# Performance work log

Measured on AMD Instinct MI355X. Metric: run time of the kernel, lower is better.

The kernel has to match this reference:

```python
import jax, jax.numpy as jnp
import numpy as np

BN_EPS = 1e-5


def grid_sample_bilinear(img, grid):
    """Torch F.grid_sample, mode=bilinear, padding_mode=zeros, align_corners=False.
    img: (B, C, H, W); grid: (B, N, 2) in [-1, 1] -> (B, C, N)."""
    B, C, H, W = img.shape
    x = ((grid[..., 0] + 1.0) * W - 1.0) * 0.5  # (B, N) pixel coords
    y = ((grid[..., 1] + 1.0) * H - 1.0) * 0.5
    x0 = jnp.floor(x)
    y0 = jnp.floor(y)
    x1 = x0 + 1.0
    y1 = y0 + 1.0
    wx1 = x - x0
    wx0 = 1.0 - wx1
    wy1 = y - y0
    wy0 = 1.0 - wy1
    img_flat = img.reshape(B, C, H * W)

    def corner(xi, yi, w):
        valid = (xi >= 0) & (xi <= W - 1) & (yi >= 0) & (yi <= H - 1)
        xi_c = jnp.clip(xi, 0, W - 1).astype(jnp.int32)
        yi_c = jnp.clip(yi, 0, H - 1).astype(jnp.int32)
        idx = yi_c * W + xi_c  # (B, N)
        vals = jnp.take_along_axis(img_flat, idx[:, None, :], axis=2)  # (B, C, N)
        return vals * (w * valid.astype(img.dtype))[:, None, :]

    return (corner(x0, y0, wx0 * wy0) + corner(x1, y0, wx1 * wy0)
            + corner(x0, y1, wx0 * wy1) + corner(x1, y1, wx1 * wy1))


def conv1x1(x, w, b):
    # x: (B, Cin, N), w: (Cout, Cin), b: (Cout,)
    return jnp.einsum('oi,bin->bon', w, x) + b[None, :, None]


def batchnorm1d_train(x, gamma, beta):
    # training-mode BN over (batch, length) per channel, biased variance
    mean = jnp.mean(x, axis=(0, 2), keepdims=True)
    var = jnp.mean((x - mean) ** 2, axis=(0, 2), keepdims=True)
    xn = (x - mean) * jax.lax.rsqrt(var + BN_EPS)
    return xn * gamma[None, :, None] + beta[None, :, None]


def setup_inputs() -> dict:
    key = jax.random.key(0)
    ks = jax.random.split(key, 12)
    B, N, CI, CP, H, W, R = 4, 16384, 256, 256, 64, 160, 4
    Cin = CI + CP
    Cb = CP // R

    def glorot(k, shape):
        fan_in = shape[1]
        return jax.random.normal(k, shape, dtype=jnp.float32) * (1.0 / np.sqrt(fan_in))

    return {
        'pts_img': jax.random.uniform(ks[0], (B, N, 2), dtype=jnp.float32, minval=-1.0, maxval=1.0),
        'img_feats': jax.random.normal(ks[1], (B, CI, H, W), dtype=jnp.float32),
        'pts_feats': jax.random.normal(ks[2], (B, CP, N), dtype=jnp.float32),
        'fusion_w': glorot(ks[3], (CP, Cin)),
        'fusion_b': jax.random.normal(ks[4], (CP,), dtype=jnp.float32) * 0.01,
        'bn_gamma': jnp.ones((CP,), dtype=jnp.float32),
        'bn_beta': jnp.zeros((CP,), dtype=jnp.float32),
        'ca1_w': glorot(ks[5], (Cb, CP)),
        'ca1_b': jax.random.normal(ks[6], (Cb,), dtype=jnp.float32) * 0.01,
        'ca2_w': glorot(ks[7], (CP, Cb)),
        'ca2_b': jax.random.normal(ks[8], (CP,), dtype=jnp.float32) * 0.01,
        'sa_w': glorot(ks[9], (Cb, CP)),
        'sa_b': jax.random.normal(ks[10], (Cb,), dtype=jnp.float32) * 0.01,
    }


def reference(pts_img, img_feats, pts_feats, fusion_w, fusion_b, bn_gamma, bn_beta,
              ca1_w, ca1_b, ca2_w, ca2_b, sa_w, sa_b):
    # grid_sample gather: (B, C_I, N)
    pts_wise_img_feats = grid_sample_bilinear(img_feats, pts_img)
    fusion = jnp.concatenate([pts_wise_img_feats, pts_feats], axis=1)  # (B, C_I+C_P, N)
    # fusion MLP: conv1x1 + BN + ReLU
    fusion = jax.nn.relu(batchnorm1d_train(conv1x1(fusion, fusion_w, fusion_b), bn_gamma, bn_beta))
    # spatial attention: max over channels of bottleneck conv, sigmoid gate
    spatial = jax.nn.sigmoid(jnp.max(conv1x1(fusion, sa_w, sa_b), axis=1, keepdims=True))
    fusion = spatial * fusion
    # channel attention: bottleneck MLP, global max-pool over points, sigmoid gate
    ca = conv1x1(jax.nn.relu(conv1x1(fusion, ca1_w, ca1_b)), ca2_w, ca2_b)  # (B, C_P, N)
    channel = jax.nn.sigmoid(jnp.max(ca, axis=2, keepdims=True))  # (B, C_P, 1)
    return channel * fusion
```

## Files before the change

### kernel.cpp

```cpp
#include <hip/hip_runtime.h>
#include <stdint.h>


typedef __attribute__((ext_vector_type(8))) short bf16x8;
typedef __attribute__((ext_vector_type(4))) float f32x4;

#define B_ 4
#define N_ 16384
#define H_ 64
#define W_ 160
#define HW_ (H_ * W_)
#define K_ 512

__device__ __forceinline__ float bf2f(unsigned short u) {
    union { unsigned int i; float f; } c; c.i = ((unsigned int)u) << 16; return c.f;
}
__device__ __forceinline__ unsigned short f2bf(float f) {
    union { float f; unsigned int i; } c; c.f = f;
    unsigned int u = c.i;
    return (unsigned short)((u + 0x7FFFu + ((u >> 16) & 1u)) >> 16);
}
__device__ __forceinline__ unsigned int fkey(float f) {
    union { float f; unsigned int u; int i; } c; c.f = f;
    return (c.i < 0) ? ~c.u : (c.u | 0x80000000u);
}
__device__ __forceinline__ float funkey(unsigned int k) {
    union { unsigned int u; float f; } c;
    c.u = (k & 0x80000000u) ? (k & 0x7FFFFFFFu) : ~k;
    return c.f;
}

__device__ __forceinline__ void async_copy16(void* lds, const void* g) {
#if defined(__has_builtin) && __has_builtin(__builtin_amdgcn_global_load_lds)
    __builtin_amdgcn_global_load_lds(
        (const __attribute__((address_space(1))) unsigned int*)g,
        (__attribute__((address_space(3))) unsigned int*)lds, 16, 0, 0);
#else
    *(uint4*)lds = *(const uint4*)g;
#endif
}

__global__ __launch_bounds__(256) void k_init(const float* __restrict__ fw,
                                              const float* __restrict__ saw,
                                              const float* __restrict__ c1w,
                                              const float* __restrict__ c2w,
                                              unsigned short* WfB, unsigned short* saB,
                                              unsigned short* ca1B, unsigned short* ca2B,
                                              float* buckets, unsigned int* camax) {
    int t = threadIdx.x;
    int j = blockIdx.x;
    if (j == 0) {
        for (int i = t; i < 16 * 512; i += 256) buckets[i] = 0.f;
        for (int i = t; i < 8 * 1024; i += 256) camax[i] = 0u;
    }
    int i = j * 256 + t;
    if (i < 131072) WfB[i] = f2bf(fw[i]);
    else if (i < 147456) saB[i - 131072] = f2bf(saw[i - 131072]);
    else if (i < 163840) ca1B[i - 147456] = f2bf(c1w[i - 147456]);
    else if (i < 180224) ca2B[i - 163840] = f2bf(c2w[i - 163840]);
}

__global__ __launch_bounds__(256, 3) void k_zimg(const unsigned short* __restrict__ WfB,
                                                 const float* __restrict__ img,
                                                 unsigned short* __restrict__ ZT) {
    __shared__ __align__(16) char smem[21504];
    unsigned short* At = (unsigned short*)smem;
    unsigned short* Bt = (unsigned short*)(smem + 16384);

    int t = threadIdx.x;
    int hw0 = blockIdx.x * 64, b = blockIdx.y;
    int w = t >> 6, lane = t & 63, quad = lane >> 4, l15 = lane & 15;

    const f32x4 fzero = {0.f, 0.f, 0.f, 0.f};
    f32x4 acc[4][4];
#pragma unroll
    for (int i = 0; i < 4; ++i)
#pragma unroll
        for (int j = 0; j < 4; ++j) acc[i][j] = fzero;

    for (int kt = 0; kt < 8; ++kt) {
        int k0 = kt * 32;
        __syncthreads();
#pragma unroll
        for (int q = 0; q < 4; ++q) {
            int row = q * 64 + (t >> 2);
            async_copy16(At + (size_t)q * 2048 + (size_t)t * 8,
                         WfB + (size_t)row * K_ + k0 + (t & 3) * 8);
        }
        {
            int c_local = t & 31, g = t >> 5;
            int c = k0 + c_local;
            const float* src = img + ((size_t)b * 256 + c) * (size_t)HW_ + hw0 + g * 8;
            float4 v0 = *(const float4*)(src + 0);
            float4 v1 = *(const float4*)(src + 4);
            unsigned short* dst = Bt + (size_t)(g * 8) * 40 + c_local;
            dst[0 * 40] = f2bf(v0.x); dst[1 * 40] = f2bf(v0.y);
            dst[2 * 40] = f2bf(v0.z); dst[3 * 40] = f2bf(v0.w);
            dst[4 * 40] = f2bf(v1.x); dst[5 * 40] = f2bf(v1.y);
            dst[6 * 40] = f2bf(v1.z); dst[7 * 40] = f2bf(v1.w);
        }
        __syncthreads();
        bf16x8 af[4], bv[4];
#pragma unroll
        for (int j = 0; j < 4; ++j)
            bv[j] = *(const bf16x8*)(Bt + (j * 16 + l15) * 40 + quad * 8);
#pragma unroll
        for (int i = 0; i < 4; ++i)
            af[i] = *(const bf16x8*)(At + (w * 64 + i * 16 + l15) * 32 + quad * 8);
#pragma unroll
        for (int i = 0; i < 4; ++i)
#pragma unroll
            for (int j = 0; j < 4; ++j)
                acc[i][j] = __builtin_amdgcn_mfma_f32_16x16x32_bf16(af[i], bv[j], acc[i][j], 0, 0, 0);
    }

    unsigned short* Zb = ZT + ((size_t)b * HW_ + hw0) * 256;
#pragma unroll
    for (int i = 0; i < 4; ++i) {
        int m = w * 64 + i * 16 + quad * 4;
#pragma unroll
        for (int j = 0; j < 4; ++j) {
            int n = j * 16 + l15;
            ushort4 o;
            o.x = f2bf(acc[i][j][0]);
            o.y = f2bf(acc[i][j][1]);
            o.z = f2bf(acc[i][j][2]);
            o.w = f2bf(acc[i][j][3]);
            *(ushort4*)(Zb + (size_t)n * 256 + m) = o;
        }
    }
}

__global__ __launch_bounds__(256, 2) void k_gemm1p(const unsigned short* __restrict__ WfB,
                                                   const float* __restrict__ pim,
                                                   const unsigned short* __restrict__ ZT,
                                                   const float* __restrict__ pts,
                                                   const float* __restrict__ fb,
                                                   unsigned short* __restrict__ Y,
                                                   float* __restrict__ buckets) {
    __shared__ __align__(16) char smem[41984];
    unsigned short* At = (unsigned short*)smem;
    unsigned short* Bt = (unsigned short*)(smem + 16384);
    unsigned short* tile = (unsigned short*)smem;
    float* biasS = (float*)(smem + 34816);
    float* redS  = (float*)(smem + 35840);
    float* redQ  = (float*)(smem + 36864);
    uint4*  offs4 = (uint4*)(smem + 37888);
    float4* wts4  = (float4*)(smem + 39936);

    int t = threadIdx.x;
    int n0 = blockIdx.x * 128, bb = blockIdx.y;
    int w = t >> 6, lane = t & 63, quad = lane >> 4, l15 = lane & 15;
    const unsigned short* Zb = ZT + (size_t)bb * HW_ * 256;

    if (t < 128) {
        float2 g2 = *(const float2*)(pim + (size_t)((size_t)bb * N_ + n0 + t) * 2);
        float x = (g2.x + 1.0f) * (0.5f * W_) - 0.5f;
        float y = (g2.y + 1.0f) * (0.5f * H_) - 0.5f;
        float xf = floorf(x), yf = floorf(y);
        float wx1 = x - xf, wx0 = 1.0f - wx1;
        float wy1 = y - yf, wy0 = 1.0f - wy1;
        int x0 = (int)xf, y0 = (int)yf;
        int x1 = x0 + 1, y1 = y0 + 1;
        float vx0 = (x0 >= 0 && x0 < W_) ? 1.f : 0.f;
        float vx1 = (x1 >= 0 && x1 < W_) ? 1.f : 0.f;
        float vy0 = (y0 >= 0 && y0 < H_) ? 1.f : 0.f;
        float vy1 = (y1 >= 0 && y1 < H_) ? 1.f : 0.f;
        int cx0 = min(max(x0, 0), W_ - 1), cx1 = min(max(x1, 0), W_ - 1);
        int cy0 = min(max(y0, 0), H_ - 1), cy1 = min(max(y1, 0), H_ - 1);
        uint4 o4;
        o4.x = (unsigned)(cy0 * W_ + cx0);
        o4.y = (unsigned)(cy0 * W_ + cx1);
        o4.z = (unsigned)(cy1 * W_ + cx0);
        o4.w = (unsigned)(cy1 * W_ + cx1);
        offs4[t] = o4;
        float4 w4;
        w4.x = wx0 * wy0 * vx0 * vy0;
        w4.y = wx1 * wy0 * vx1 * vy0;
        w4.z = wx0 * wy1 * vx0 * vy1;
        w4.w = wx1 * wy1 * vx1 * vy1;
        wts4[t] = w4;
    }
    biasS[t] = fb[t];

    const f32x4 fzero = {0.f, 0.f, 0.f, 0.f};
    f32x4 acc[4][8];
#pragma unroll
    for (int i = 0; i < 4; ++i)
#pragma unroll
        for (int j = 0; j < 8; ++j) acc[i][j] = fzero;

    for (int kt = 0; kt < 8; ++kt) {
        int k0 = kt * 32;
        __syncthreads();
#pragma unroll
        for (int q = 0; q < 4; ++q) {
            int row = q * 64 + (t >> 2);
            async_copy16(At + (size_t)q * 2048 + (size_t)t * 8,
                         WfB + (size_t)row * K_ + 256 + k0 + (t & 3) * 8);
        }
        {
            int c_local = t & 31, g = t >> 5;
            int c = k0 + c_local;
            const float* src = pts + ((size_t)bb * 256 + c) * (size_t)N_ + n0 + g * 16;
            float4 v0 = *(const float4*)(src + 0);
            float4 v1 = *(const float4*)(src + 4);
            float4 v2 = *(const float4*)(src + 8);
            float4 v3 = *(const float4*)(src + 12);
            unsigned short* dst = Bt + (size_t)g * 16 * 40 + c_local;
            dst[0 * 40] = f2bf(v0.x); dst[1 * 40] = f2bf(v0.y);
            dst[2 * 40] = f2bf(v0.z); dst[3 * 40] = f2bf(v0.w);
            dst[4 * 40] = f2bf(v1.x); dst[5 * 40] = f2bf(v1.y);
            dst[6 * 40] = f2bf(v1.z); dst[7 * 40] = f2bf(v1.w);
            dst[8 * 40] = f2bf(v2.x); dst[9 * 40] = f2bf(v2.y);
            dst[10 * 40] = f2bf(v2.z); dst[11 * 40] = f2bf(v2.w);
            dst[12 * 40] = f2bf(v3.x); dst[13 * 40] = f2bf(v3.y);
            dst[14 * 40] = f2bf(v3.z); dst[15 * 40] = f2bf(v3.w);
        }
        __syncthreads();
        bf16x8 af[4], bv[8];
#pragma unroll
        for (int j = 0; j < 8; ++j)
            bv[j] = *(const bf16x8*)(Bt + (j * 16 + l15) * 40 + quad * 8);
#pragma unroll
        for (int i = 0; i < 4; ++i)
            af[i] = *(const bf16x8*)(At + (w * 64 + i * 16 + l15) * 32 + quad * 8);
#pragma unroll
        for (int i = 0; i < 4; ++i)
#pragma unroll
            for (int j = 0; j < 8; ++j)
                acc[i][j] = __builtin_amdgcn_mfma_f32_16x16x32_bf16(af[i], bv[j], acc[i][j], 0, 0, 0);
    }

    __syncthreads();

    size_t Yrow0 = ((size_t)bb * N_ + n0) * 256;
#pragma unroll
    for (int h = 0; h < 2; ++h) {
        if (h == 1) __syncthreads();
        {
            int pt = t >> 1;
            uint4 o4 = offs4[pt];
            float4 w4 = wts4[pt];
            const unsigned short* pA = Zb + (size_t)o4.x * 256;
            const unsigned short* pB = Zb + (size_t)o4.y * 256;
            const unsigned short* pC = Zb + (size_t)o4.z * 256;
            const unsigned short* pD = Zb + (size_t)o4.w * 256;
            int mbase = h * 128 + (t & 1) * 64;
            int lbase = (t & 1) * 64;
#pragma unroll
            for (int s = 0; s < 8; ++s) {
                int mc = mbase + s * 8;
                uint4 cA = *(const uint4*)(pA + mc);
                uint4 cB = *(const uint4*)(pB + mc);
                uint4 cC = *(const uint4*)(pC + mc);
                uint4 cD = *(const uint4*)(pD + mc);
                const unsigned short* qa = (const unsigned short*)&cA;
                const unsigned short* qb = (const unsigned short*)&cB;
                const unsigned short* qc = (const unsigned short*)&cC;
                const unsigned short* qd = (const unsigned short*)&cD;
                uint4 ov;
                unsigned short* po = (unsigned short*)&ov;
#pragma unroll
                for (int e = 0; e < 8; ++e)
                    po[e] = f2bf(w4.x * bf2f(qa[e]) + w4.y * bf2f(qb[e]) +
                                 w4.z * bf2f(qc[e]) + w4.w * bf2f(qd[e]));
                *(uint4*)(tile + pt * 136 + lbase + s * 8) = ov;
            }
        }
        __syncthreads();
        if ((w >> 1) == h) {
            int hw = w & 1;
#pragma unroll
            for (int i = 0; i < 4; ++i) {
                int mloc = hw * 64 + i * 16 + quad * 4;
                int mg = h * 128 + mloc;
                float b0 = biasS[mg + 0], b1 = biasS[mg + 1];
                float b2 = biasS[mg + 2], b3 = biasS[mg + 3];
                float s0 = 0.f, q0 = 0.f, s1 = 0.f, q1 = 0.f;
                float s2 = 0.f, q2 = 0.f, s3 = 0.f, q3 = 0.f;
#pragma unroll
                for (int j = 0; j < 8; ++j) {
                    int n = j * 16 + l15;
                    ushort4 v = *(const ushort4*)(tile + n * 136 + mloc);
                    float y0 = acc[i][j][0] + bf2f(v.x) + b0;
                    float y1 = acc[i][j][1] + bf2f(v.y) + b1;
                    float y2 = acc[i][j][2] + bf2f(v.z) + b2;
                    float y3 = acc[i][j][3] + bf2f(v.w) + b3;
                    s0 += y0; q0 += y0 * y0;
                    s1 += y1; q1 += y1 * y1;
                    s2 += y2; q2 += y2 * y2;
                    s3 += y3; q3 += y3 * y3;
                    ushort4 o;
                    o.x = f2bf(y0); o.y = f2bf(y1); o.z = f2bf(y2); o.w = f2bf(y3);
                    *(ushort4*)(tile + n * 136 + mloc) = o;
                }
#pragma unroll
                for (int d = 1; d < 16; d <<= 1) {
                    s0 += __shfl_xor(s0, d, 64); q0 += __shfl_xor(q0, d, 64);
                    s1 += __shfl_xor(s1, d, 64); q1 += __shfl_xor(q1, d, 64);
                    s2 += __shfl_xor(s2, d, 64); q2 += __shfl_xor(q2, d, 64);
                    s3 += __shfl_xor(s3, d, 64); q3 += __shfl_xor(q3, d, 64);
                }
                if (l15 == 0) {
                    redS[mg + 0] = s0; redQ[mg + 0] = q0;
                    redS[mg + 1] = s1; redQ[mg + 1] = q1;
                    redS[mg + 2] = s2; redQ[mg + 2] = q2;
                    redS[mg + 3] = s3; redQ[mg + 3] = q3;
                }
            }
        }
        __syncthreads();
        if (t < 128) {
            float* bk = buckets + (size_t)(blockIdx.x & 15) * 512;
            atomicAdd(bk + h * 128 + t, redS[h * 128 + t]);
            atomicAdd(bk + 256 + h * 128 + t, redQ[h * 128 + t]);
        }
#pragma unroll
        for (int pass = 0; pass < 8; ++pass) {
            int row = pass * 16 + (t >> 4);
            int cB2 = (t & 15) * 8;
            uint4 v = *(const uint4*)(tile + row * 136 + cB2);
            *(uint4*)(Y + Yrow0 + (size_t)row * 256 + h * 128 + cB2) = v;
        }
    }
}

__global__ __launch_bounds__(256, 2) void k_gate(const unsigned short* __restrict__ Y,
                                                 const float* __restrict__ buckets,
                                                 const float* __restrict__ gamma,
                                                 const float* __restrict__ beta,
                                                 const unsigned short* __restrict__ saB,
                                                 const float* __restrict__ sab,
                                                 const unsigned short* __restrict__ c1B,
                                                 const float* __restrict__ c1b,
                                                 const unsigned short* __restrict__ c2B,
                                                 unsigned int* __restrict__ camax,
                                                 float* __restrict__ sp_g,
                                                 float* __restrict__ ss_out) {
    __shared__ __align__(16) unsigned short Ft[64 * 264];
    __shared__ __align__(16) unsigned short Ht[64 * 72];
    __shared__ float scS[256], shS[256];
    __shared__ float saPart[4][64];
    __shared__ float spL[64];
    int t = threadIdx.x;
    size_t pts0 = (size_t)blockIdx.x * 64;
    int b = (int)(pts0 >> 14);
    int w = t >> 6, lane = t & 63, quad = lane >> 4, l15 = lane & 15;
    int jrow = w * 16 + l15;

    bf16x8 bvs[8], bvc[8];
#pragma unroll
    for (int kt = 0; kt < 8; ++kt) {
        bvs[kt] = *(const bf16x8*)(saB + (size_t)jrow * 256 + kt * 32 + quad * 8);
        bvc[kt] = *(const bf16x8*)(c1B + (size_t)jrow * 256 + kt * 32 + quad * 8);
    }
    float sbias = sab[jrow];
    float cbias = c1b[jrow];

    {
        float s = 0.f, q = 0.f;
#pragma unroll
        for (int bk = 0; bk < 16; ++bk) {
            s += buckets[bk * 512 + t];
            q += buckets[bk * 512 + 256 + t];
        }
        const float inv = 1.0f / (float)(B_ * N_);
        float mean = s * inv;
        float var = q * inv - mean * mean;
        float sc = gamma[t] * rsqrtf(var + 1e-5f);
        float sh = beta[t] - mean * sc;
        scS[t] = sc;
        shS[t] = sh;
        if (blockIdx.x == 0) { ss_out[t] = sc; ss_out[256 + t] = sh; }
    }
    __syncthreads();

    int cc = (t * 8) & 255;
    float scr[8], shr[8];
#pragma unroll
    for (int e = 0; e < 8; ++e) { scr[e] = scS[cc + e]; shr[e] = shS[cc + e]; }
    for (int idx = t * 8; idx < 64 * 256; idx += 2048) {
        int r = idx >> 8;
        uint4 v = *(const uint4*)(Y + (pts0 + r) * 256 + cc);
        unsigned short* us = (unsigned short*)&v;
#pragma unroll
        for (int e = 0; e < 8; ++e) {
            float f = bf2f(us[e]) * scr[e] + shr[e];
            us[e] = f2bf(fmaxf(f, 0.f));
        }
        *(uint4*)(Ft + r * 264 + cc) = v;
    }
    __syncthreads();

    const f32x4 fzero = {0.f, 0.f, 0.f, 0.f};
    f32x4 accS[4], accC[4];
#pragma unroll
    for (int i = 0; i < 4; ++i) { accS[i] = fzero; accC[i] = fzero; }
#pragma unroll
    for (int kt = 0; kt < 8; ++kt) {
        bf16x8 af[4];
#pragma unroll
        for (int i = 0; i < 4; ++i)
            af[i] = *(const bf16x8*)(Ft + (i * 16 + l15) * 264 + kt * 32 + quad * 8);
#pragma unroll
        for (int i = 0; i < 4; ++i) {
            accS[i] = __builtin_amdgcn_mfma_f32_16x16x32_bf16(af[i], bvs[kt], accS[i], 0, 0, 0);
            accC[i] = __builtin_amdgcn_mfma_f32_16x16x32_bf16(af[i], bvc[kt], accC[i], 0, 0, 0);
        }
    }
#pragma unroll
    for (int i = 0; i < 4; ++i) {
#pragma unroll
        for (int r = 0; r < 4; ++r) {
            float v = accS[i][r] + sbias;
#pragma unroll
            for (int d = 1; d < 16; d <<= 1) v = fmaxf(v, __shfl_xor(v, d, 64));
            if (l15 == 0) saPart[w][i * 16 + quad * 4 + r] = v;
        }
    }
    __syncthreads();
    if (t < 64) {
        float m4 = fmaxf(fmaxf(saPart[0][t], saPart[1][t]),
                         fmaxf(saPart[2][t], saPart[3][t]));
        float sv = 1.0f / (1.0f + __expf(-m4));
        spL[t] = sv;
        sp_g[pts0 + t] = sv;
    }
    __syncthreads();

#pragma unroll
    for (int i = 0; i < 4; ++i) {
#pragma unroll
        for (int r = 0; r < 4; ++r) {
            int pt = i * 16 + quad * 4 + r;
            float hv = fmaxf(accC[i][r] * spL[pt] + cbias, 0.f);
            Ht[pt * 72 + jrow] = f2bf(hv);
        }
    }
    __syncthreads();

    {
        bf16x8 b2a[4], b2b[4];
#pragma unroll
        for (int mt = 0; mt < 4; ++mt) {
            b2a[mt] = *(const bf16x8*)(c2B + (size_t)(w * 64 + mt * 16 + l15) * 64 + quad * 8);
            b2b[mt] = *(const bf16x8*)(c2B + (size_t)(w * 64 + mt * 16 + l15) * 64 + 32 + quad * 8);
        }
        float vmax[4] = {-3e38f, -3e38f, -3e38f, -3e38f};
#pragma unroll
        for (int i = 0; i < 4; ++i) {
            bf16x8 a0 = *(const bf16x8*)(Ht + (i * 16 + l15) * 72 + quad * 8);
            bf16x8 a1 = *(const bf16x8*)(Ht + (i * 16 + l15) * 72 + 32 + quad * 8);
#pragma unroll
            for (int mt = 0; mt < 4; ++mt) {
                f32x4 acc = __builtin_amdgcn_mfma_f32_16x16x32_bf16(a0, b2a[mt], fzero, 0, 0, 0);
                acc = __builtin_amdgcn_mfma_f32_16x16x32_bf16(a1, b2b[mt], acc, 0, 0, 0);
#pragma unroll
                for (int r = 0; r < 4; ++r) vmax[mt] = fmaxf(vmax[mt], acc[r]);
            }
        }
        unsigned int* cam = camax + (size_t)(blockIdx.x & 7) * 1024 + b * 256;
#pragma unroll
        for (int mt = 0; mt < 4; ++mt) {
            float v = vmax[mt];
            v = fmaxf(v, __shfl_xor(v, 16, 64));
            v = fmaxf(v, __shfl_xor(v, 32, 64));
            if (quad == 0) atomicMax(cam + w * 64 + mt * 16 + l15, fkey(v));
        }
    }
}

__global__ __launch_bounds__(256) void k_out(const unsigned short* __restrict__ Y,
                                             const unsigned int* __restrict__ camax,
                                             const float* __restrict__ c2b,
                                             const float* __restrict__ ss,
                                             const float* __restrict__ sp_g,
                                             float* __restrict__ out) {
    __shared__ __align__(16) unsigned short tile[64 * 68];
    __shared__ float ch[64], scT[64], shT[64], spT[64];
    int t = threadIdx.x;
    int n0 = blockIdx.x * 64, m0 = blockIdx.y * 64, b = blockIdx.z;
    if (t < 64) {
        int m = m0 + t;
        unsigned int k = 0u;
#pragma unroll
        for (int bk = 0; bk < 8; ++bk) k = max(k, camax[bk * 1024 + b * 256 + m]);
        ch[t] = 1.0f / (1.0f + __expf(-(funkey(k) + c2b[m])));
        scT[t] = ss[m];
        shT[t] = ss[256 + m];
        spT[t] = sp_g[(size_t)b * N_ + n0 + t];
    }
    int sub = (t & 15) * 4, grp = t >> 4;
    const unsigned short* src = Y + ((size_t)b * N_ + n0) * 256 + m0;
#pragma unroll
    for (int it = 0; it < 4; ++it) {
        int nl = grp + it * 16;
        ushort4 v = *(const ushort4*)(src + (size_t)nl * 256 + sub);
        *(ushort4*)(tile + nl * 68 + sub) = v;
    }
    __syncthreads();
    float* dst = out + ((size_t)b * 256 + m0) * N_ + n0;
#pragma unroll
    for (int it = 0; it < 4; ++it) {
        int ml = grp + it * 16;
        float g = ch[ml], scv = scT[ml], shv = shT[ml];
        float4 o;
        o.x = fmaxf(bf2f(tile[(sub + 0) * 68 + ml]) * scv + shv, 0.f) * spT[sub + 0] * g;
        o.y = fmaxf(bf2f(tile[(sub + 1) * 68 + ml]) * scv + shv, 0.f) * spT[sub + 1] * g;
        o.z = fmaxf(bf2f(tile[(sub + 2) * 68 + ml]) * scv + shv, 0.f) * spT[sub + 2] * g;
        o.w = fmaxf(bf2f(tile[(sub + 3) * 68 + ml]) * scv + shv, 0.f) * spT[sub + 3] * g;
        *(float4*)(dst + (size_t)ml * N_ + sub) = o;
    }
}

extern "C" void kernel_launch(void* const* d_in, const int* in_sizes, int n_in,
                              void* d_out, int out_size, void* d_ws, size_t ws_size,
                              hipStream_t stream) {
    (void)in_sizes; (void)n_in; (void)out_size; (void)ws_size;
    const float* pts_img = (const float*)d_in[0];
    const float* img     = (const float*)d_in[1];
    const float* pts     = (const float*)d_in[2];
    const float* fw      = (const float*)d_in[3];
    const float* fbias   = (const float*)d_in[4];
    const float* gamma   = (const float*)d_in[5];
    const float* beta    = (const float*)d_in[6];
    const float* c1w     = (const float*)d_in[7];
    const float* c1b     = (const float*)d_in[8];
    const float* c2w     = (const float*)d_in[9];
    const float* c2b     = (const float*)d_in[10];
    const float* saw     = (const float*)d_in[11];
    const float* sab     = (const float*)d_in[12];
    float* out = (float*)d_out;

    char* ws = (char*)d_ws;
    unsigned short* ZT   = (unsigned short*)(ws);
    unsigned short* Y    = (unsigned short*)(ws + 20971520);
    unsigned short* WfB  = (unsigned short*)(ws + 54525952);
    unsigned short* saB  = (unsigned short*)(ws + 54788096);
    unsigned short* ca1B = (unsigned short*)(ws + 54820864);
    unsigned short* ca2B = (unsigned short*)(ws + 54853632);
    float* buckets       = (float*)(ws + 54886400);
    unsigned int* camax  = (unsigned int*)(ws + 54919168);
    float* sp_g          = (float*)(ws + 54951936);
    float* ss            = (float*)(ws + 55214080);

    k_init<<<704, 256, 0, stream>>>(fw, saw, c1w, c2w, WfB, saB, ca1B, ca2B, buckets, camax);
    k_zimg<<<dim3(160, 4), 256, 0, stream>>>(WfB, img, ZT);
    k_gemm1p<<<dim3(128, 4), 256, 0, stream>>>(WfB, pts_img, ZT, pts, fbias, Y, buckets);
    k_gate<<<1024, 256, 0, stream>>>(Y, buckets, gamma, beta, saB, sab, ca1B, c1b,
                                     ca2B, camax, sp_g, ss);
    k_out<<<dim3(256, 4, 4), 256, 0, stream>>>(Y, camax, c2b, ss, sp_g, out);
}
```

Baseline: 280.5 us.

## Halve gemm1p point tile and stage k_zimg output through LDS

```diff
diff --git a/kernel.cpp b/kernel.cpp
--- a/kernel.cpp
+++ b/kernel.cpp
@@ -63,9 +63,10 @@
 __global__ __launch_bounds__(256, 3) void k_zimg(const unsigned short* __restrict__ WfB,
                                                  const float* __restrict__ img,
                                                  unsigned short* __restrict__ ZT) {
-    __shared__ __align__(16) char smem[21504];
+    __shared__ __align__(16) char smem[33792];
     unsigned short* At = (unsigned short*)smem;
     unsigned short* Bt = (unsigned short*)(smem + 16384);
+    unsigned short* tile = (unsigned short*)smem;
 
     int t = threadIdx.x;
     int hw0 = blockIdx.x * 64, b = blockIdx.y;
@@ -114,7 +115,7 @@
                 acc[i][j] = __builtin_amdgcn_mfma_f32_16x16x32_bf16(af[i], bv[j], acc[i][j], 0, 0, 0);
     }
 
-    unsigned short* Zb = ZT + ((size_t)b * HW_ + hw0) * 256;
+    __syncthreads();
 #pragma unroll
     for (int i = 0; i < 4; ++i) {
         int m = w * 64 + i * 16 + quad * 4;
@@ -126,34 +127,42 @@
             o.y = f2bf(acc[i][j][1]);
             o.z = f2bf(acc[i][j][2]);
             o.w = f2bf(acc[i][j][3]);
-            *(ushort4*)(Zb + (size_t)n * 256 + m) = o;
-        }
-    }
-}
-
-__global__ __launch_bounds__(256, 2) void k_gemm1p(const unsigned short* __restrict__ WfB,
+            *(ushort4*)(tile + n * 264 + m) = o;
+        }
+    }
+    __syncthreads();
+    unsigned short* Zb = ZT + ((size_t)b * HW_ + hw0) * 256;
+#pragma unroll
+    for (int pass = 0; pass < 8; ++pass) {
+        int row = pass * 8 + (t >> 5);
+        int col = (t & 31) * 8;
+        *(uint4*)(Zb + (size_t)row * 256 + col) = *(const uint4*)(tile + row * 264 + col);
+    }
+}
+
+__global__ __launch_bounds__(256, 4) void k_gemm1p(const unsigned short* __restrict__ WfB,
                                                    const float* __restrict__ pim,
                                                    const unsigned short* __restrict__ ZT,
                                                    const float* __restrict__ pts,
                                                    const float* __restrict__ fb,
                                                    unsigned short* __restrict__ Y,
                                                    float* __restrict__ buckets) {
-    __shared__ __align__(16) char smem[41984];
+    __shared__ __align__(16) char smem[38912];
     unsigned short* At = (unsigned short*)smem;
     unsigned short* Bt = (unsigned short*)(smem + 16384);
     unsigned short* tile = (unsigned short*)smem;
-    float* biasS = (float*)(smem + 34816);
-    float* redS  = (float*)(smem + 35840);
-    float* redQ  = (float*)(smem + 36864);
-    uint4*  offs4 = (uint4*)(smem + 37888);
-    float4* wts4  = (float4*)(smem + 39936);
+    uint4*  offs4 = (uint4*)(smem + 33792);
+    float4* wts4  = (float4*)(smem + 34816);
+    float* biasS = (float*)(smem + 35840);
+    float* redS  = (float*)(smem + 36864);
+    float* redQ  = (float*)(smem + 37888);
 
     int t = threadIdx.x;
-    int n0 = blockIdx.x * 128, bb = blockIdx.y;
+    int n0 = blockIdx.x * 64, bb = blockIdx.y;
     int w = t >> 6, lane = t & 63, quad = lane >> 4, l15 = lane & 15;
     const unsigned short* Zb = ZT + (size_t)bb * HW_ * 256;
 
-    if (t < 128) {
+    if (t < 64) {
         float2 g2 = *(const float2*)(pim + (size_t)((size_t)bb * N_ + n0 + t) * 2);
         float x = (g2.x + 1.0f) * (0.5f * W_) - 0.5f;
         float y = (g2.y + 1.0f) * (0.5f * H_) - 0.5f;
@@ -184,11 +193,11 @@
     biasS[t] = fb[t];
 
     const f32x4 fzero = {0.f, 0.f, 0.f, 0.f};
-    f32x4 acc[4][8];
+    f32x4 acc[4][4];
 #pragma unroll
     for (int i = 0; i < 4; ++i)
 #pragma unroll
-        for (int j = 0; j < 8; ++j) acc[i][j] = fzero;
+        for (int j = 0; j < 4; ++j) acc[i][j] = fzero;
 
     for (int kt = 0; kt < 8; ++kt) {
         int k0 = kt * 32;
@@ -202,25 +211,19 @@
         {
             int c_local = t & 31, g = t >> 5;
             int c = k0 + c_local;
-            const float* src = pts + ((size_t)bb * 256 + c) * (size_t)N_ + n0 + g * 16;
+            const float* src = pts + ((size_t)bb * 256 + c) * (size_t)N_ + n0 + g * 8;
             float4 v0 = *(const float4*)(src + 0);
             float4 v1 = *(const float4*)(src + 4);
-            float4 v2 = *(const float4*)(src + 8);
-            float4 v3 = *(const float4*)(src + 12);
-            unsigned short* dst = Bt + (size_t)g * 16 * 40 + c_local;
+            unsigned short* dst = Bt + (size_t)(g * 8) * 40 + c_local;
             dst[0 * 40] = f2bf(v0.x); dst[1 * 40] = f2bf(v0.y);
             dst[2 * 40] = f2bf(v0.z); dst[3 * 40] = f2bf(v0.w);
             dst[4 * 40] = f2bf(v1.x); dst[5 * 40] = f2bf(v1.y);
             dst[6 * 40] = f2bf(v1.z); dst[7 * 40] = f2bf(v1.w);
-            dst[8 * 40] = f2bf(v2.x); dst[9 * 40] = f2bf(v2.y);
-            dst[10 * 40] = f2bf(v2.z); dst[11 * 40] = f2bf(v2.w);
-            dst[12 * 40] = f2bf(v3.x); dst[13 * 40] = f2bf(v3.y);
-            dst[14 * 40] = f2bf(v3.z); dst[15 * 40] = f2bf(v3.w);
         }
         __syncthreads();
-        bf16x8 af[4], bv[8];
-#pragma unroll
-        for (int j = 0; j < 8; ++j)
+        bf16x8 af[4], bv[4];
+#pragma unroll
+        for (int j = 0; j < 4; ++j)
             bv[j] = *(const bf16x8*)(Bt + (j * 16 + l15) * 40 + quad * 8);
 #pragma unroll
         for (int i = 0; i < 4; ++i)
@@ -228,101 +231,90 @@
 #pragma unroll
         for (int i = 0; i < 4; ++i)
 #pragma unroll
-            for (int j = 0; j < 8; ++j)
+            for (int j = 0; j < 4; ++j)
                 acc[i][j] = __builtin_amdgcn_mfma_f32_16x16x32_bf16(af[i], bv[j], acc[i][j], 0, 0, 0);
     }
 
     __syncthreads();
 
+    {
+        int pt = t >> 2, q = t & 3;
+        uint4 o4 = offs4[pt];
+        float4 w4 = wts4[pt];
+        const unsigned short* pA = Zb + (size_t)o4.x * 256;
+        const unsigned short* pB = Zb + (size_t)o4.y * 256;
+        const unsigned short* pC = Zb + (size_t)o4.z * 256;
+        const unsigned short* pD = Zb + (size_t)o4.w * 256;
+#pragma unroll
+        for (int s = 0; s < 8; ++s) {
+            int mc = q * 64 + s * 8;
+            uint4 cA = *(const uint4*)(pA + mc);
+            uint4 cB = *(const uint4*)(pB + mc);
+            uint4 cC = *(const uint4*)(pC + mc);
+            uint4 cD = *(const uint4*)(pD + mc);
+            const unsigned short* qa = (const unsigned short*)&cA;
+            const unsigned short* qb = (const unsigned short*)&cB;
+            const unsigned short* qc = (const unsigned short*)&cC;
+            const unsigned short* qd = (const unsigned short*)&cD;
+            uint4 ov;
+            unsigned short* po = (unsigned short*)&ov;
+#pragma unroll
+            for (int e = 0; e < 8; ++e)
+                po[e] = f2bf(w4.x * bf2f(qa[e]) + w4.y * bf2f(qb[e]) +
+                             w4.z * bf2f(qc[e]) + w4.w * bf2f(qd[e]));
+            *(uint4*)(tile + pt * 264 + mc) = ov;
+        }
+    }
+    __syncthreads();
+#pragma unroll
+    for (int i = 0; i < 4; ++i) {
+        int mloc = w * 64 + i * 16 + quad * 4;
+        float b0 = biasS[mloc + 0], b1 = biasS[mloc + 1];
+        float b2 = biasS[mloc + 2], b3 = biasS[mloc + 3];
+        float s0 = 0.f, q0 = 0.f, s1 = 0.f, q1 = 0.f;
+        float s2 = 0.f, q2 = 0.f, s3 = 0.f, q3 = 0.f;
+#pragma unroll
+        for (int j = 0; j < 4; ++j) {
+            int n = j * 16 + l15;
+            ushort4 v = *(const ushort4*)(tile + n * 264 + mloc);
+            float y0 = acc[i][j][0] + bf2f(v.x) + b0;
+            float y1 = acc[i][j][1] + bf2f(v.y) + b1;
+            float y2 = acc[i][j][2] + bf2f(v.z) + b2;
+            float y3 = acc[i][j][3] + bf2f(v.w) + b3;
+            s0 += y0; q0 += y0 * y0;
+            s1 += y1; q1 += y1 * y1;
+            s2 += y2; q2 += y2 * y2;
+            s3 += y3; q3 += y3 * y3;
+            ushort4 o;
+            o.x = f2bf(y0); o.y = f2bf(y1); o.z = f2bf(y2); o.w = f2bf(y3);
+            *(ushort4*)(tile + n * 264 + mloc) = o;
+        }
+#pragma unroll
+        for (int d = 1; d < 16; d <<= 1) {
+            s0 += __shfl_xor(s0, d, 64); q0 += __shfl_xor(q0, d, 64);
+            s1 += __shfl_xor(s1, d, 64); q1 += __shfl_xor(q1, d, 64);
+            s2 += __shfl_xor(s2, d, 64); q2 += __shfl_xor(q2, d, 64);
+            s3 += __shfl_xor(s3, d, 64); q3 += __shfl_xor(q3, d, 64);
+        }
+        if (l15 == 0) {
+            redS[mloc + 0] = s0; redQ[mloc + 0] = q0;
+            redS[mloc + 1] = s1; redQ[mloc + 1] = q1;
+            redS[mloc + 2] = s2; redQ[mloc + 2] = q2;
+            redS[mloc + 3] = s3; redQ[mloc + 3] = q3;
+        }
+    }
+    __syncthreads();
+    {
+        float* bk = buckets + (size_t)(blockIdx.x & 15) * 512;
+        atomicAdd(bk + t, redS[t]);
+        atomicAdd(bk + 256 + t, redQ[t]);
+    }
     size_t Yrow0 = ((size_t)bb * N_ + n0) * 256;
 #pragma unroll
-    for (int h = 0; h < 2; ++h) {
-        if (h == 1) __syncthreads();
-        {
-            int pt = t >> 1;
-            uint4 o4 = offs4[pt];
-            float4 w4 = wts4[pt];
-            const unsigned short* pA = Zb + (size_t)o4.x * 256;
-            const unsigned short* pB = Zb + (size_t)o4.y * 256;
-            const unsigned short* pC = Zb + (size_t)o4.z * 256;
-            const unsigned short* pD = Zb + (size_t)o4.w * 256;
-            int mbase = h * 128 + (t & 1) * 64;
-            int lbase = (t & 1) * 64;
-#pragma unroll
-            for (int s = 0; s < 8; ++s) {
-                int mc = mbase + s * 8;
-                uint4 cA = *(const uint4*)(pA + mc);
-                uint4 cB = *(const uint4*)(pB + mc);
-                uint4 cC = *(const uint4*)(pC + mc);
-                uint4 cD = *(const uint4*)(pD + mc);
-                const unsigned short* qa = (const unsigned short*)&cA;
-                const unsigned short* qb = (const unsigned short*)&cB;
-                const unsigned short* qc = (const unsigned short*)&cC;
-                const unsigned short* qd = (const unsigned short*)&cD;
-                uint4 ov;
-                unsigned short* po = (unsigned short*)&ov;
-#pragma unroll
-                for (int e = 0; e < 8; ++e)
-                    po[e] = f2bf(w4.x * bf2f(qa[e]) + w4.y * bf2f(qb[e]) +
-                                 w4.z * bf2f(qc[e]) + w4.w * bf2f(qd[e]));
-                *(uint4*)(tile + pt * 136 + lbase + s * 8) = ov;
-            }
-        }
-        __syncthreads();
-        if ((w >> 1) == h) {
-            int hw = w & 1;
-#pragma unroll
-            for (int i = 0; i < 4; ++i) {
-                int mloc = hw * 64 + i * 16 + quad * 4;
-                int mg = h * 128 + mloc;
-                float b0 = biasS[mg + 0], b1 = biasS[mg + 1];
-                float b2 = biasS[mg + 2], b3 = biasS[mg + 3];
-                float s0 = 0.f, q0 = 0.f, s1 = 0.f, q1 = 0.f;
-                float s2 = 0.f, q2 = 0.f, s3 = 0.f, q3 = 0.f;
-#pragma unroll
-                for (int j = 0; j < 8; ++j) {
-                    int n = j * 16 + l15;
-                    ushort4 v = *(const ushort4*)(tile + n * 136 + mloc);
-                    float y0 = acc[i][j][0] + bf2f(v.x) + b0;
-                    float y1 = acc[i][j][1] + bf2f(v.y) + b1;
-                    float y2 = acc[i][j][2] + bf2f(v.z) + b2;
-                    float y3 = acc[i][j][3] + bf2f(v.w) + b3;
-                    s0 += y0; q0 += y0 * y0;
-                    s1 += y1; q1 += y1 * y1;
-                    s2 += y2; q2 += y2 * y2;
-                    s3 += y3; q3 += y3 * y3;
-                    ushort4 o;
-                    o.x = f2bf(y0); o.y = f2bf(y1); o.z = f2bf(y2); o.w = f2bf(y3);
-                    *(ushort4*)(tile + n * 136 + mloc) = o;
-                }
-#pragma unroll
-                for (int d = 1; d < 16; d <<= 1) {
-                    s0 += __shfl_xor(s0, d, 64); q0 += __shfl_xor(q0, d, 64);
-                    s1 += __shfl_xor(s1, d, 64); q1 += __shfl_xor(q1, d, 64);
-                    s2 += __shfl_xor(s2, d, 64); q2 += __shfl_xor(q2, d, 64);
-                    s3 += __shfl_xor(s3, d, 64); q3 += __shfl_xor(q3, d, 64);
-                }
-                if (l15 == 0) {
-                    redS[mg + 0] = s0; redQ[mg + 0] = q0;
-                    redS[mg + 1] = s1; redQ[mg + 1] = q1;
-                    redS[mg + 2] = s2; redQ[mg + 2] = q2;
-                    redS[mg + 3] = s3; redQ[mg + 3] = q3;
-                }
-            }
-        }
-        __syncthreads();
-        if (t < 128) {
-            float* bk = buckets + (size_t)(blockIdx.x & 15) * 512;
-            atomicAdd(bk + h * 128 + t, redS[h * 128 + t]);
-            atomicAdd(bk + 256 + h * 128 + t, redQ[h * 128 + t]);
-        }
-#pragma unroll
-        for (int pass = 0; pass < 8; ++pass) {
-            int row = pass * 16 + (t >> 4);
-            int cB2 = (t & 15) * 8;
-            uint4 v = *(const uint4*)(tile + row * 136 + cB2);
-            *(uint4*)(Y + Yrow0 + (size_t)row * 256 + h * 128 + cB2) = v;
-        }
+    for (int pass = 0; pass < 8; ++pass) {
+        int row = pass * 8 + (t >> 5);
+        int col = (t & 31) * 8;
+        *(uint4*)(Y + Yrow0 + (size_t)row * 256 + col) = *(const uint4*)(tile + row * 264 + col);
     }
 }
 
@@ -547,7 +539,7 @@
 
     k_init<<<704, 256, 0, stream>>>(fw, saw, c1w, c2w, WfB, saB, ca1B, ca2B, buckets, camax);
     k_zimg<<<dim3(160, 4), 256, 0, stream>>>(WfB, img, ZT);
-    k_gemm1p<<<dim3(128, 4), 256, 0, stream>>>(WfB, pts_img, ZT, pts, fbias, Y, buckets);
+    k_gemm1p<<<dim3(256, 4), 256, 0, stream>>>(WfB, pts_img, ZT, pts, fbias, Y, buckets);
     k_gate<<<1024, 256, 0, stream>>>(Y, buckets, gamma, beta, saB, sab, ca1B, c1b,
                                      ca2B, camax, sp_g, ss);
     k_out<<<dim3(256, 4, 4), 256, 0, stream>>>(Y, camax, c2b, ss, sp_g, out);
```

Result: slower. 299.9 us (+6.9%).
